# Kernel tuning notes

Measured on AMD Instinct MI355X. Metric: run time of the kernel, lower is better.

The kernel has to match this reference:

```python
import jax, jax.numpy as jnp
import numpy as np

B = 2048          # batch_size
D = 512           # embedding dim
TEMP = 0.1        # temperature
EPS = 1e-8        # torch CosineSimilarity eps


def _neg_idx(batch_size):
    n = 2 * batch_size
    mask = np.eye(n) + np.eye(n, n, k=-batch_size) + np.eye(n, n, k=batch_size)
    mask = (1 - mask).astype(bool)           # True at negatives
    # each row has exactly n-2 True entries -> fixed-shape gather indices
    return np.nonzero(mask)[1].reshape(n, n - 2)

_NEG_IDX = jnp.asarray(_neg_idx(B))           # [2B, 2B-2]
_ROWS = jnp.arange(2 * B)[:, None]            # [2B, 1]


def _cos_sim_matrix(r):
    # r: [2B, D] -> [2B, 2B] cosine similarity
    norm = jnp.maximum(jnp.linalg.norm(r, axis=-1, keepdims=True), EPS)
    rn = r / norm
    return rn @ rn.T


def _pos(sim):
    # diag(sim, +B) and diag(sim, -B), concatenated -> [2B, 1]
    l = jnp.diagonal(sim, offset=B)
    r = jnp.diagonal(sim, offset=-B)
    return jnp.concatenate([l, r])[:, None]


def _neg(sim):
    # masked gather of off-(diag,+B,-B) entries -> [2B, 2B-2]
    return sim[_ROWS, _NEG_IDX]


def _ce_sum_label0(logits):
    # CrossEntropyLoss(reduction='sum') with all labels == 0
    return -jnp.sum(jax.nn.log_softmax(logits, axis=-1)[:, 0])


def setup_inputs() -> dict:
    key = jax.random.key(0)
    k1, k2, k3, k4 = jax.random.split(key, 4)
    return {
        "z_ori": jax.random.normal(k1, (B, D), jnp.float32),
        "z_hard_pos": jax.random.normal(k2, (B, D), jnp.float32),
        "z_soft_pos": jax.random.normal(k3, (B, D), jnp.float32),
        "z_soft_neg": jax.random.normal(k4, (B, D), jnp.float32),
    }


def reference(z_ori, z_hard_pos, z_soft_pos, z_soft_neg):
    sim_ori_hp = _cos_sim_matrix(jnp.concatenate([z_ori, z_hard_pos], axis=0))
    sim_ori_sp = _cos_sim_matrix(jnp.concatenate([z_ori, z_soft_pos], axis=0))
    sim_ori_sn = _cos_sim_matrix(jnp.concatenate([z_ori, z_soft_neg], axis=0))
    sim_hp_sp = _cos_sim_matrix(jnp.concatenate([z_hard_pos, z_soft_pos], axis=0))
    sim_hp_sn = _cos_sim_matrix(jnp.concatenate([z_hard_pos, z_soft_neg], axis=0))
    sim_sp_sn = _cos_sim_matrix(jnp.concatenate([z_soft_pos, z_soft_neg], axis=0))

    pos_ori_sn = _pos(sim_ori_sn)
    pos_hp_sn = _pos(sim_hp_sn)
    pos_sp_sn = _pos(sim_sp_sn)

    pos_ori_hp = _pos(sim_ori_hp)
    neg_ori_hp = _neg(sim_ori_hp)
    pos_ori_sp = _pos(sim_ori_sp)
    neg_ori_sp = _neg(sim_ori_sp)
    pos_hp_sp = _pos(sim_hp_sp)
    neg_hp_sp = _neg(sim_hp_sp)

    logits_ori_hp = jnp.concatenate([pos_ori_hp, neg_ori_hp, pos_ori_sn], axis=1) / TEMP
    logits_ori_sp = jnp.concatenate([pos_ori_sp, neg_ori_sp, pos_ori_sn], axis=1) / TEMP
    logits_hp_sp = jnp.concatenate([pos_hp_sp, neg_hp_sp, pos_hp_sn, pos_sp_sn], axis=1) / TEMP

    denom = 2.0 * B
    return (
        _ce_sum_label0(logits_ori_hp) / denom,
        _ce_sum_label0(logits_ori_sp) / denom,
        _ce_sum_label0(logits_hp_sp) / denom,
    )
```

## Files before the change

### kernel.cpp

```cpp
#include <hip/hip_runtime.h>
#include <hip/hip_bf16.h>

#define Bn 2048
#define Dn 512

typedef float f32x4 __attribute__((ext_vector_type(4)));
typedef long long ll2 __attribute__((ext_vector_type(2)));

typedef __attribute__((address_space(1))) const unsigned int gas_u32;
typedef __attribute__((address_space(3))) unsigned int las_u32;

__device__ __forceinline__ void gload16(const void* g, void* l) {
  __builtin_amdgcn_global_load_lds((gas_u32*)g, (las_u32*)l, 16, 0, 0);
}

__global__ __launch_bounds__(256) void normalize_kernel(
    const float* __restrict__ in0, const float* __restrict__ in1,
    const float* __restrict__ in2, const float* __restrict__ in3,
    unsigned char* __restrict__ nm8, float* __restrict__ rs, float* __restrict__ dd,
    float* __restrict__ out) {
  __shared__ float sv[4][Dn];
  __shared__ float red[4][6];
  int row = blockIdx.x;
  int wave = threadIdx.x >> 6, lane = threadIdx.x & 63;

  int g0 = blockIdx.x * 256 + threadIdx.x;
  if (g0 < 9 * Bn) rs[g0] = 0.0f;
  if (g0 < 3) out[g0] = 0.0f;

  const float* src =
      (wave == 0 ? in0 : wave == 1 ? in1 : wave == 2 ? in2 : in3) + (size_t)row * Dn;
  int k = lane * 8;
  float4 x0 = *(const float4*)(src + k);
  float4 x1 = *(const float4*)(src + k + 4);
  float v[8] = {x0.x, x0.y, x0.z, x0.w, x1.x, x1.y, x1.z, x1.w};
  float ss = 0.f;
#pragma unroll
  for (int e = 0; e < 8; e++) ss = fmaf(v[e], v[e], ss);
#pragma unroll
  for (int off = 1; off < 64; off <<= 1) ss += __shfl_xor(ss, off, 64);
  float scale = 1.0f / fmaxf(sqrtf(ss), 1e-8f);
  float nv[8];
#pragma unroll
  for (int e = 0; e < 8; e++) {
    nv[e] = v[e] * scale;
    sv[wave][k + e] = nv[e];
  }
  if (wave < 3) {
    unsigned int lo = __builtin_amdgcn_cvt_pk_fp8_f32(nv[0], nv[1], 0u, false);
    lo = __builtin_amdgcn_cvt_pk_fp8_f32(nv[2], nv[3], lo, true);
    unsigned int hi = __builtin_amdgcn_cvt_pk_fp8_f32(nv[4], nv[5], 0u, false);
    hi = __builtin_amdgcn_cvt_pk_fp8_f32(nv[6], nv[7], hi, true);
    uint2 pk; pk.x = lo; pk.y = hi;
    int kb = lane >> 3, g = lane & 7;
    int p = ((g & 3) << 1) | (g >> 2);
    *(uint2*)(nm8 + ((size_t)wave * Bn + row) * Dn + kb * 64 + p * 8) = pk;
  }
  __syncthreads();

  int t = threadIdx.x;
  float o0 = sv[0][2 * t], o1 = sv[0][2 * t + 1];
  float h0 = sv[1][2 * t], h1 = sv[1][2 * t + 1];
  float p0 = sv[2][2 * t], p1 = sv[2][2 * t + 1];
  float n0 = sv[3][2 * t], n1 = sv[3][2 * t + 1];
  float s[6];
  s[0] = fmaf(o0, h0, o1 * h1);
  s[1] = fmaf(o0, p0, o1 * p1);
  s[2] = fmaf(h0, p0, h1 * p1);
  s[3] = fmaf(o0, n0, o1 * n1);
  s[4] = fmaf(h0, n0, h1 * n1);
  s[5] = fmaf(p0, n0, p1 * n1);
#pragma unroll
  for (int off = 1; off < 64; off <<= 1) {
#pragma unroll
    for (int j = 0; j < 6; j++) s[j] += __shfl_xor(s[j], off, 64);
  }
  if (lane == 0) {
#pragma unroll
    for (int j = 0; j < 6; j++) red[wave][j] = s[j];
  }
  __syncthreads();
  if (threadIdx.x < 6) {
    int j = threadIdx.x;
    dd[j * Bn + row] = red[0][j] + red[1][j] + red[2][j] + red[3][j];
  }
}

#define GBM 128
#define GBK 64
#define NKT 8
#define NBUF 3

__global__ __launch_bounds__(512, 6) void gemm_fp8_kernel(const unsigned char* __restrict__ nm8,
                                                          float* __restrict__ rs) {
  __shared__ unsigned char lds[NBUF * 16384];

  int id = ((int)blockIdx.x & 7) * 147 + ((int)blockIdx.x >> 3);
  int by = 0, rem = id, cnt = 48;
  while (rem >= cnt) { rem -= cnt; by++; cnt--; }
  int bx = by + rem;
  int u = by >> 4, v = bx >> 4;
  int rrow, rcol;
  if (u == v) { rrow = u; rcol = u; }
  else if (u == 0) { if (v == 1) { rrow = 3; rcol = 4; } else { rrow = 5; rcol = 6; } }
  else { rrow = 7; rcol = 8; }

  const unsigned char* gA = nm8 + ((size_t)u * Bn + (size_t)(by & 15) * GBM) * Dn;
  const unsigned char* gB = nm8 + ((size_t)v * Bn + (size_t)(bx & 15) * GBM) * Dn;

  int tid = threadIdx.x, lane = tid & 63, wave = tid >> 6;
  int wr = wave >> 2, wc = wave & 3;
  int c = lane & 15, rgrp = lane >> 4;
  int ru = ((rgrp ^ ((c >> 1) & 3)) << 4);

  int srow = tid >> 2;
  int suu = (tid & 3) ^ ((srow >> 1) & 3);
  size_t aoff = (size_t)srow * Dn + suu * 16;
  const unsigned char* sA = gA + aoff;
  const unsigned char* sB = gB + aoff;
  int dbase = wave << 10;

#define STAGE(kt, j)                                         \
  {                                                          \
    unsigned char* d = lds + (j) * 16384;                    \
    gload16(sA + (kt) * GBK, d + dbase);                     \
    gload16(sB + (kt) * GBK, d + 8192 + dbase);              \
  }

  f32x4 acc[4][2] = {};

  STAGE(0, 0);
  STAGE(1, 1);
  asm volatile("s_waitcnt vmcnt(2)" ::: "memory");
  __builtin_amdgcn_s_barrier();
  asm volatile("" ::: "memory");

#pragma unroll
  for (int t = 0; t < NKT; ++t) {
    const unsigned char* As = lds + (t % 3) * 16384;
    const unsigned char* Bs = As + 8192;
    if (t + 2 < NKT) STAGE(t + 2, (t + 2) % 3);
    ll2 a[4];
    ll2 b[2];
#pragma unroll
    for (int mi = 0; mi < 4; ++mi)
      a[mi] = *(const ll2*)(As + (wr * 64 + mi * 16 + c) * 64 + ru);
#pragma unroll
    for (int ni = 0; ni < 2; ++ni)
      b[ni] = *(const ll2*)(Bs + (wc * 32 + ni * 16 + c) * 64 + ru);
    __builtin_amdgcn_s_setprio(1);
#pragma unroll
    for (int ks = 0; ks < 2; ++ks)
#pragma unroll
      for (int mi = 0; mi < 4; ++mi)
#pragma unroll
        for (int ni = 0; ni < 2; ++ni)
          acc[mi][ni] = __builtin_amdgcn_mfma_f32_16x16x32_fp8_fp8(
              a[mi][ks], b[ni][ks], acc[mi][ni], 0, 0, 0);
    __builtin_amdgcn_s_setprio(0);
    if (t + 2 < NKT) {
      asm volatile("s_waitcnt vmcnt(2)" ::: "memory");
    } else if (t + 1 < NKT) {
      asm volatile("s_waitcnt vmcnt(0)" ::: "memory");
    }
    __builtin_amdgcn_s_barrier();
    asm volatile("" ::: "memory");
    __builtin_amdgcn_sched_barrier(0);
  }
#undef STAGE

  float* crow = (float*)lds;
  float* ccol = crow + GBM;
  __syncthreads();
  if (tid < 2 * GBM) ((float*)lds)[tid] = 0.0f;
  __syncthreads();

  bool skip_diag = (by == bx);
#pragma unroll
  for (int mi = 0; mi < 4; ++mi)
#pragma unroll
    for (int ni = 0; ni < 2; ++ni)
#pragma unroll
      for (int r = 0; r < 4; ++r) {
        int lrow = wr * 64 + mi * 16 + rgrp * 4 + r;
        int lcol = wc * 32 + ni * 16 + c;
        float e = __expf(10.0f * acc[mi][ni][r] - 10.0f);
        acc[mi][ni][r] = (skip_diag && lrow == lcol) ? 0.0f : e;
      }

#pragma unroll
  for (int mi = 0; mi < 4; ++mi)
#pragma unroll
    for (int r = 0; r < 4; ++r) {
      float val = acc[mi][0][r] + acc[mi][1][r];
      val += __shfl_xor(val, 1, 64);
      val += __shfl_xor(val, 2, 64);
      val += __shfl_xor(val, 4, 64);
      val += __shfl_xor(val, 8, 64);
      if (c == 0) atomicAdd(&crow[wr * 64 + mi * 16 + rgrp * 4 + r], val);
    }
#pragma unroll
  for (int ni = 0; ni < 2; ++ni) {
    float cv = 0.f;
#pragma unroll
    for (int mi = 0; mi < 4; ++mi)
#pragma unroll
      for (int r = 0; r < 4; ++r) cv += acc[mi][ni][r];
    cv += __shfl_xor(cv, 16, 64);
    cv += __shfl_xor(cv, 32, 64);
    if (lane < 16) atomicAdd(&ccol[wc * 32 + ni * 16 + c], cv);
  }
  __syncthreads();

  float* rs_row = rs + rrow * Bn + (by & 15) * GBM;
  if (tid < GBM) {
    atomicAdd(rs_row + tid, crow[tid]);
  } else if (tid < 2 * GBM && by != bx) {
    float* rs_col = rs + rcol * Bn + (bx & 15) * GBM;
    atomicAdd(rs_col + (tid - GBM), ccol[tid - GBM]);
  }
}

__global__ __launch_bounds__(256) void final_kernel(const float* __restrict__ rs,
                                                    const float* __restrict__ dd,
                                                    float* __restrict__ out) {
  int i = blockIdx.x * 256 + threadIdx.x;
  float doh = dd[i], dop = dd[Bn + i], dhp = dd[2 * Bn + i];
  float ea = __expf(10.0f * dd[3 * Bn + i] - 10.0f);
  float eb = __expf(10.0f * dd[4 * Bn + i] - 10.0f);
  float ec = __expf(10.0f * dd[5 * Bn + i] - 10.0f);
  float r0 = rs[i], r1 = rs[Bn + i], r2 = rs[2 * Bn + i];
  float r3 = rs[3 * Bn + i], r4 = rs[4 * Bn + i], r5 = rs[5 * Bn + i];
  float r6 = rs[6 * Bn + i], r7 = rs[7 * Bn + i], r8 = rs[8 * Bn + i];
  float l1 = 20.0f + logf(r0 + r3 + ea) + logf(r4 + r1 + ea) - 20.0f * doh;
  float l2 = 20.0f + logf(r0 + r5 + ea) + logf(r6 + r2 + ea) - 20.0f * dop;
  float l3 = 20.0f + logf(r1 + r7 + eb + ec) + logf(r8 + r2 + eb + ec) - 20.0f * dhp;

  __shared__ float red[3][256];
  int tid = threadIdx.x;
  red[0][tid] = l1; red[1][tid] = l2; red[2][tid] = l3;
  __syncthreads();
  for (int s = 128; s > 0; s >>= 1) {
    if (tid < s) {
      red[0][tid] += red[0][tid + s];
      red[1][tid] += red[1][tid + s];
      red[2][tid] += red[2][tid + s];
    }
    __syncthreads();
  }
  if (tid < 3) atomicAdd(&out[tid], red[tid][0] * (1.0f / 4096.0f));
}

extern "C" void kernel_launch(void* const* d_in, const int* in_sizes, int n_in,
                              void* d_out, int out_size, void* d_ws, size_t ws_size,
                              hipStream_t stream) {
  const float* z0 = (const float*)d_in[0];
  const float* z1 = (const float*)d_in[1];
  const float* z2 = (const float*)d_in[2];
  const float* z3 = (const float*)d_in[3];
  float* out = (float*)d_out;

  unsigned char* nm8 = (unsigned char*)d_ws;
  float* rs = (float*)((char*)d_ws + (size_t)3 * Bn * Dn);
  float* dd = rs + 9 * Bn;

  hipLaunchKernelGGL(normalize_kernel, dim3(2048), dim3(256), 0, stream,
                     z0, z1, z2, z3, nm8, rs, dd, out);
  hipLaunchKernelGGL(gemm_fp8_kernel, dim3(1176), dim3(512), 0, stream, nm8, rs);
  hipLaunchKernelGGL(final_kernel, dim3(8), dim3(256), 0, stream, rs, dd, out);
}
```

Measured before the change: 39.94 us.

## Switch GEMM tile MFMA from 16x16x32 to 32x32x16 fp8

Replaces the 4x2 grid of 16x16x32 fp8 MFMAs per wave with two 32x32x16 fp8 MFMAs per k-substep. The fp8 byte permutation in the normalize kernel, the LDS read swizzle and the row/column reduction epilogue are all rewritten to match the new operand and accumulator layout. The goal is fewer LDS fragment loads and fewer MFMA issues per unit of work. The cost is a 16-lane shuffle reduction per accumulator register and a riskier register layout to get right.

```diff
diff --git a/kernel.cpp b/kernel.cpp
--- a/kernel.cpp
+++ b/kernel.cpp
@@ -4,7 +4,7 @@
 #define Bn 2048
 #define Dn 512
 
-typedef float f32x4 __attribute__((ext_vector_type(4)));
+typedef float f32x16 __attribute__((ext_vector_type(16)));
 typedef long long ll2 __attribute__((ext_vector_type(2)));
 
 typedef __attribute__((address_space(1))) const unsigned int gas_u32;
@@ -53,7 +53,7 @@
     hi = __builtin_amdgcn_cvt_pk_fp8_f32(nv[6], nv[7], hi, true);
     uint2 pk; pk.x = lo; pk.y = hi;
     int kb = lane >> 3, g = lane & 7;
-    int p = ((g & 3) << 1) | (g >> 2);
+    int p = (g & 4) | ((g & 1) << 1) | ((g >> 1) & 1);
     *(uint2*)(nm8 + ((size_t)wave * Bn + row) * Dn + kb * 64 + p * 8) = pk;
   }
   __syncthreads();
@@ -110,8 +110,10 @@
 
   int tid = threadIdx.x, lane = tid & 63, wave = tid >> 6;
   int wr = wave >> 2, wc = wave & 3;
-  int c = lane & 15, rgrp = lane >> 4;
-  int ru = ((rgrp ^ ((c >> 1) & 3)) << 4);
+  int r = lane & 31, h = lane >> 5;
+  int swz = (r >> 1) & 3;
+  int u0 = ((h ^ swz) << 4);
+  int u1 = (((2 + h) ^ swz) << 4);
 
   int srow = tid >> 2;
   int suu = (tid & 3) ^ ((srow >> 1) & 3);
@@ -127,7 +129,7 @@
     gload16(sB + (kt) * GBK, d + 8192 + dbase);              \
   }
 
-  f32x4 acc[4][2] = {};
+  f32x16 acc[2] = {};
 
   STAGE(0, 0);
   STAGE(1, 1);
@@ -140,23 +142,25 @@
     const unsigned char* As = lds + (t % 3) * 16384;
     const unsigned char* Bs = As + 8192;
     if (t + 2 < NKT) STAGE(t + 2, (t + 2) % 3);
-    ll2 a[4];
-    ll2 b[2];
-#pragma unroll
-    for (int mi = 0; mi < 4; ++mi)
-      a[mi] = *(const ll2*)(As + (wr * 64 + mi * 16 + c) * 64 + ru);
-#pragma unroll
-    for (int ni = 0; ni < 2; ++ni)
-      b[ni] = *(const ll2*)(Bs + (wc * 32 + ni * 16 + c) * 64 + ru);
+    ll2 a[2][2], b[2];
+#pragma unroll
+    for (int mi = 0; mi < 2; ++mi) {
+      int rbase = (wr * 64 + mi * 32 + r) * 64;
+      a[mi][0] = *(const ll2*)(As + rbase + u0);
+      a[mi][1] = *(const ll2*)(As + rbase + u1);
+    }
+    {
+      int rbase = (wc * 32 + r) * 64;
+      b[0] = *(const ll2*)(Bs + rbase + u0);
+      b[1] = *(const ll2*)(Bs + rbase + u1);
+    }
     __builtin_amdgcn_s_setprio(1);
 #pragma unroll
-    for (int ks = 0; ks < 2; ++ks)
-#pragma unroll
-      for (int mi = 0; mi < 4; ++mi)
-#pragma unroll
-        for (int ni = 0; ni < 2; ++ni)
-          acc[mi][ni] = __builtin_amdgcn_mfma_f32_16x16x32_fp8_fp8(
-              a[mi][ks], b[ni][ks], acc[mi][ni], 0, 0, 0);
+    for (int s = 0; s < 4; ++s)
+#pragma unroll
+      for (int mi = 0; mi < 2; ++mi)
+        acc[mi] = __builtin_amdgcn_mfma_f32_32x32x16_fp8_fp8(
+            a[mi][s >> 1][s & 1], b[s >> 1][s & 1], acc[mi], 0, 0, 0);
     __builtin_amdgcn_s_setprio(0);
     if (t + 2 < NKT) {
       asm volatile("s_waitcnt vmcnt(2)" ::: "memory");
@@ -176,39 +180,37 @@
   __syncthreads();
 
   bool skip_diag = (by == bx);
-#pragma unroll
-  for (int mi = 0; mi < 4; ++mi)
-#pragma unroll
-    for (int ni = 0; ni < 2; ++ni)
-#pragma unroll
-      for (int r = 0; r < 4; ++r) {
-        int lrow = wr * 64 + mi * 16 + rgrp * 4 + r;
-        int lcol = wc * 32 + ni * 16 + c;
-        float e = __expf(10.0f * acc[mi][ni][r] - 10.0f);
-        acc[mi][ni][r] = (skip_diag && lrow == lcol) ? 0.0f : e;
-      }
-
-#pragma unroll
-  for (int mi = 0; mi < 4; ++mi)
-#pragma unroll
-    for (int r = 0; r < 4; ++r) {
-      float val = acc[mi][0][r] + acc[mi][1][r];
+  int lcol = wc * 32 + r;
+#pragma unroll
+  for (int mi = 0; mi < 2; ++mi)
+#pragma unroll
+    for (int reg = 0; reg < 16; ++reg) {
+      int lrow = wr * 64 + mi * 32 + (reg & 3) + 8 * (reg >> 2) + 4 * h;
+      float e = __expf(10.0f * acc[mi][reg] - 10.0f);
+      acc[mi][reg] = (skip_diag && lrow == lcol) ? 0.0f : e;
+    }
+
+#pragma unroll
+  for (int mi = 0; mi < 2; ++mi)
+#pragma unroll
+    for (int reg = 0; reg < 16; ++reg) {
+      float val = acc[mi][reg];
       val += __shfl_xor(val, 1, 64);
       val += __shfl_xor(val, 2, 64);
       val += __shfl_xor(val, 4, 64);
       val += __shfl_xor(val, 8, 64);
-      if (c == 0) atomicAdd(&crow[wr * 64 + mi * 16 + rgrp * 4 + r], val);
-    }
-#pragma unroll
-  for (int ni = 0; ni < 2; ++ni) {
+      val += __shfl_xor(val, 16, 64);
+      if (r == 0)
+        atomicAdd(&crow[wr * 64 + mi * 32 + (reg & 3) + 8 * (reg >> 2) + 4 * h], val);
+    }
+  {
     float cv = 0.f;
 #pragma unroll
-    for (int mi = 0; mi < 4; ++mi)
-#pragma unroll
-      for (int r = 0; r < 4; ++r) cv += acc[mi][ni][r];
-    cv += __shfl_xor(cv, 16, 64);
+    for (int mi = 0; mi < 2; ++mi)
+#pragma unroll
+      for (int reg = 0; reg < 16; ++reg) cv += acc[mi][reg];
     cv += __shfl_xor(cv, 32, 64);
-    if (lane < 16) atomicAdd(&ccol[wc * 32 + ni * 16 + c], cv);
+    if (h == 0) atomicAdd(&ccol[lcol], cv);
   }
   __syncthreads();
 
```

New measurement: 52.42 us. 1.31x slower.
